# Performance work log

Hardware: AMD Instinct MI355X
Metric: run time of the kernel (lower is better)

The kernel has to match this reference:

```python
import jax, jax.numpy as jnp
import numpy as np


def _three_nn_interp(xyz1, xyz2, feat2):
    # squared Euclidean distances via gram trick, avoids (B,N,S,3) tensor
    # d2: (B, N, S)
    n1 = jnp.sum(xyz1 * xyz1, axis=-1)               # (B, N)
    n2 = jnp.sum(xyz2 * xyz2, axis=-1)               # (B, S)
    d2 = n1[:, :, None] + n2[:, None, :] - 2.0 * jnp.einsum('bnc,bsc->bns', xyz1, xyz2)
    d = jnp.sqrt(jnp.maximum(d2, 0.0))
    k = min(3, xyz2.shape[1])
    neg_d, idx = jax.lax.top_k(-d, k)                # smallest k distances
    dist = jnp.maximum(-neg_d, 1e-10)               # (B, N, k)
    w = 1.0 / dist
    w = w / jnp.sum(w, axis=-1, keepdims=True)
    # gather feat2 at idx: (B, N, k, C2)
    f2 = jnp.take_along_axis(feat2[:, None, :, :], idx[..., None], axis=2)
    return jnp.sum(f2 * w[..., None], axis=2)        # (B, N, C2)


def setup_inputs() -> dict:
    key = jax.random.key(0)
    ks = jax.random.split(key, 8)
    B, N, S, C1, C2, OUT = 8, 8192, 2048, 128, 256, 256
    IN = C1 + C2
    return {
        'xyz1': jax.random.normal(ks[0], (B, N, 3), dtype=jnp.float32),
        'xyz2': jax.random.normal(ks[1], (B, S, 3), dtype=jnp.float32),
        'feat1': jax.random.normal(ks[2], (B, N, C1), dtype=jnp.float32),
        'feat2': jax.random.normal(ks[3], (B, S, C2), dtype=jnp.float32),
        'W1': jax.random.normal(ks[4], (IN, OUT), dtype=jnp.float32) * (1.0 / np.sqrt(IN)),
        'b1': jnp.zeros((OUT,), dtype=jnp.float32),
        'W2': jax.random.normal(ks[5], (OUT, OUT), dtype=jnp.float32) * (1.0 / np.sqrt(OUT)),
        'b2': jnp.zeros((OUT,), dtype=jnp.float32),
    }


def reference(xyz1, xyz2, feat1, feat2, W1, b1, W2, b2):
    if xyz2.shape[1] == 1:
        interp = jnp.broadcast_to(feat2, (feat2.shape[0], xyz1.shape[1], feat2.shape[2]))
    else:
        interp = _three_nn_interp(xyz1, xyz2, feat2)
    x = jnp.concatenate([feat1, interp], axis=-1)    # (B, N, C1+C2)
    x = jax.nn.relu(x @ W1 + b1)
    x = jax.nn.relu(x @ W2 + b2)
    return x
```

## Files before the change

### kernel.cpp

```cpp
#include <hip/hip_runtime.h>
#include <hip/hip_bf16.h>

#define BB   8
#define NN   8192
#define SS   2048
#define C1C  128
#define C2C  256
#define KIN  384
#define OUTC 256

typedef __attribute__((ext_vector_type(4))) float f32x4;
typedef __attribute__((ext_vector_type(8))) short short8;
typedef __attribute__((ext_vector_type(8))) unsigned short ushortx8;

__device__ __forceinline__ ushort f2bf(float v) {
    __hip_bfloat16 h = __float2bfloat16(v);
    return __builtin_bit_cast(ushort, h);
}

__device__ __forceinline__ float med3(float a, float b, float c) {
    return __builtin_amdgcn_fmed3f(a, b, c);
}

__global__ __launch_bounds__(1024, 8) void knn_gather_kernel(
    const float* __restrict__ xyz1, const float* __restrict__ xyz2,
    const float* __restrict__ feat2, ushort* __restrict__ interpB)
{
    __shared__ float4 sp[SS];
    __shared__ int   sIdx[128][3];
    __shared__ float sW[128][3];

    const int tid   = threadIdx.x;
    const int b     = blockIdx.x & 7;
    const int chunk = blockIdx.x >> 3;
    const int qbase = chunk << 7;

    const float* x2 = xyz2 + (size_t)b * SS * 3;
    for (int i = tid; i < SS; i += 1024) {
        float x = x2[i*3+0], y = x2[i*3+1], z = x2[i*3+2];
        sp[i] = make_float4(-2.f*x, -2.f*y, -2.f*z, x*x + y*y + z*z);
    }
    __syncthreads();

    const int g = tid >> 4;
    const int l = tid & 15;
    const int qa = qbase + g * 2;

    const float* qp = xyz1 + ((size_t)b * NN + qa) * 3;
    float px[2] = {qp[0], qp[3]};
    float py[2] = {qp[1], qp[4]};
    float pz[2] = {qp[2], qp[5]};

    float c0[2], c1[2], c2[2];
#pragma unroll
    for (int qi = 0; qi < 2; ++qi) { c0[qi] = c1[qi] = c2[qi] = 1e30f; }

    for (int jj = 0; jj < 128; jj += 4) {
        float4 P[4];
#pragma unroll
        for (int u = 0; u < 4; ++u) P[u] = sp[((jj + u) << 4) + l];
#pragma unroll
        for (int u = 0; u < 4; ++u) {
#pragma unroll
            for (int qi = 0; qi < 2; ++qi) {
                float f = fmaf(px[qi], P[u].x,
                          fmaf(py[qi], P[u].y,
                          fmaf(pz[qi], P[u].z, P[u].w)));
                c2[qi] = med3(f, c1[qi], c2[qi]);
                c1[qi] = med3(f, c0[qi], c1[qi]);
                c0[qi] = fminf(f, c0[qi]);
            }
        }
    }

#pragma unroll
    for (int m = 1; m <= 8; m <<= 1) {
#pragma unroll
        for (int qi = 0; qi < 2; ++qi) {
            float b0 = __shfl_xor(c0[qi], m);
            float b1 = __shfl_xor(c1[qi], m);
            float b2 = __shfl_xor(c2[qi], m);
            float bv[3] = {b0, b1, b2};
#pragma unroll
            for (int e = 0; e < 3; ++e) {
                float d = bv[e];
                c2[qi] = med3(d, c1[qi], c2[qi]);
                c1[qi] = med3(d, c0[qi], c1[qi]);
                c0[qi] = fminf(d, c0[qi]);
            }
        }
    }
    const float t0 = c2[0], t1 = c2[1];

    float e0[2], e1[2], e2[2];
    int   i0[2], i1[2], i2[2];
#pragma unroll
    for (int qi = 0; qi < 2; ++qi) {
        e0[qi] = e1[qi] = e2[qi] = 1e30f;
        i0[qi] = i1[qi] = i2[qi] = 0x3fffffff;
    }

    for (int jj = 0; jj < 128; jj += 4) {
        float4 P[4];
#pragma unroll
        for (int u = 0; u < 4; ++u) P[u] = sp[((jj + u) << 4) + l];
#pragma unroll
        for (int u = 0; u < 4; ++u) {
            const int s = ((jj + u) << 4) + l;
#pragma unroll
            for (int qi = 0; qi < 2; ++qi) {
                float f = fmaf(px[qi], P[u].x,
                          fmaf(py[qi], P[u].y,
                          fmaf(pz[qi], P[u].z, P[u].w)));
                float tq = qi ? t1 : t0;
                if (f <= tq) {
                    bool lt2 = (f < e2[qi]) || (f == e2[qi] && s < i2[qi]);
                    if (lt2) {
                        bool lt1 = (f < e1[qi]) || (f == e1[qi] && s < i1[qi]);
                        bool lt0 = (f < e0[qi]) || (f == e0[qi] && s < i0[qi]);
                        e2[qi] = lt1 ? e1[qi] : f;  i2[qi] = lt1 ? i1[qi] : s;
                        e1[qi] = lt0 ? e0[qi] : (lt1 ? f : e1[qi]);
                        i1[qi] = lt0 ? i0[qi] : (lt1 ? s : i1[qi]);
                        e0[qi] = lt0 ? f : e0[qi];  i0[qi] = lt0 ? s : i0[qi];
                    }
                }
            }
        }
    }

#pragma unroll
    for (int m = 1; m <= 8; m <<= 1) {
#pragma unroll
        for (int qi = 0; qi < 2; ++qi) {
            float ob0 = __shfl_xor(e0[qi], m), ob1 = __shfl_xor(e1[qi], m), ob2 = __shfl_xor(e2[qi], m);
            int   oj0 = __shfl_xor(i0[qi], m), oj1 = __shfl_xor(i1[qi], m), oj2 = __shfl_xor(i2[qi], m);
            float dv[3] = {ob0, ob1, ob2}; int iv[3] = {oj0, oj1, oj2};
#pragma unroll
            for (int e = 0; e < 3; ++e) {
                float d = dv[e]; int s = iv[e];
                bool lt2 = (d < e2[qi]) || (d == e2[qi] && s < i2[qi]);
                if (lt2) {
                    bool lt1 = (d < e1[qi]) || (d == e1[qi] && s < i1[qi]);
                    bool lt0 = (d < e0[qi]) || (d == e0[qi] && s < i0[qi]);
                    e2[qi] = lt1 ? e1[qi] : d;  i2[qi] = lt1 ? i1[qi] : s;
                    e1[qi] = lt0 ? e0[qi] : (lt1 ? d : e1[qi]);
                    i1[qi] = lt0 ? i0[qi] : (lt1 ? s : i1[qi]);
                    e0[qi] = lt0 ? d : e0[qi];  i0[qi] = lt0 ? s : i0[qi];
                }
            }
        }
    }

    if (l == 0) {
#pragma unroll
        for (int qi = 0; qi < 2; ++qi) {
            float nx = px[qi], ny = py[qi], nz = pz[qi];
            float n1 = nx*nx + ny*ny + nz*nz;
            float d0 = sqrtf(fmaxf(n1 + e0[qi], 0.f));
            float d1 = sqrtf(fmaxf(n1 + e1[qi], 0.f));
            float d2s = sqrtf(fmaxf(n1 + e2[qi], 0.f));
            float w0 = 1.f / fmaxf(d0, 1e-10f);
            float w1 = 1.f / fmaxf(d1, 1e-10f);
            float w2 = 1.f / fmaxf(d2s, 1e-10f);
            float wsum = w0 + w1 + w2;
            int qq = g * 2 + qi;
            sIdx[qq][0] = i0[qi]; sIdx[qq][1] = i1[qi]; sIdx[qq][2] = i2[qi];
            sW[qq][0] = w0 / wsum; sW[qq][1] = w1 / wsum; sW[qq][2] = w2 / wsum;
        }
    }
    __syncthreads();

    const int wid = tid >> 6, lane = tid & 63;
    for (int qq = wid; qq < 128; qq += 16) {
        int a0 = sIdx[qq][0], a1 = sIdx[qq][1], a2 = sIdx[qq][2];
        float w0 = sW[qq][0], w1 = sW[qq][1], w2 = sW[qq][2];
        const float4* r0 = (const float4*)(feat2 + ((size_t)b * SS + a0) * C2C);
        const float4* r1 = (const float4*)(feat2 + ((size_t)b * SS + a1) * C2C);
        const float4* r2 = (const float4*)(feat2 + ((size_t)b * SS + a2) * C2C);
        float4 v0 = r0[lane], v1 = r1[lane], v2 = r2[lane];
        ushort4 o;
        o.x = f2bf(w0*v0.x + w1*v1.x + w2*v2.x);
        o.y = f2bf(w0*v0.y + w1*v1.y + w2*v2.y);
        o.z = f2bf(w0*v0.z + w1*v1.z + w2*v2.z);
        o.w = f2bf(w0*v0.w + w1*v1.w + w2*v2.w);
        *(ushort4*)(interpB + ((size_t)b * NN + qbase + qq) * C2C + lane * 4) = o;
    }
}

__global__ __launch_bounds__(256) void transpose_cvt_both_kernel(
    const float* __restrict__ W1, ushort* __restrict__ W1t,
    const float* __restrict__ W2, ushort* __restrict__ W2t)
{
    int idx = blockIdx.x * 256 + threadIdx.x;
    const int n1 = KIN * OUTC;
    if (idx < n1) {
        int n = idx / KIN, k = idx - n * KIN;
        W1t[idx] = f2bf(W1[(size_t)k * OUTC + n]);
    } else {
        int j = idx - n1;
        if (j < OUTC * OUTC) {
            int n = j / OUTC, k = j - n * OUTC;
            W2t[j] = f2bf(W2[(size_t)k * OUTC + n]);
        }
    }
}

#define GBM 128
#define GBN 256
#define GBK 32

__device__ __forceinline__ void gld_lds16(const void* g, void* l) {
    __builtin_amdgcn_global_load_lds(
        (const __attribute__((address_space(1))) void*)g,
        (__attribute__((address_space(3))) void*)l, 16, 0, 0);
}

__global__ __launch_bounds__(512, 4) void gemm_fused(
    const float* __restrict__ feat1,
    const ushort* __restrict__ interpB,
    const ushort* __restrict__ W1t, const float* __restrict__ b1,
    const ushort* __restrict__ W2t, const float* __restrict__ b2,
    float* __restrict__ out)
{
    __shared__ ushort pool[GBM * 256];
    __shared__ ushort sB2[GBN * GBK];

    ushort* sA = pool;
    ushort* sB = pool + GBM * GBK;

    const int tid  = threadIdx.x;
    const int lane = tid & 63;
    const int wid  = tid >> 6;
    const int m0   = blockIdx.x * GBM;
    const int wr   = wid >> 2;
    const int wc   = wid & 3;

    const int rsub = lane >> 2;
    const int slot = lane & 3;
    const int csub = slot * 8;
    const int usw  = (slot ^ (rsub & 3)) * 8;

    const int kgrp = (lane >> 4) * 8;
    const int rl   = lane & 15;
    const int ksw  = kgrp ^ ((rl & 3) << 3);
    const int cl   = lane & 15;
    const int rgrp = (lane >> 4) * 4;

    f32x4 acc1[4][4];
#pragma unroll
    for (int i = 0; i < 4; ++i)
#pragma unroll
        for (int j = 0; j < 4; ++j) acc1[i][j] = (f32x4){0.f, 0.f, 0.f, 0.f};

    for (int k0 = 0; k0 < KIN; k0 += GBK) {
#pragma unroll
        for (int c = 0; c < 3; ++c) {
            const int cid = wid * 3 + c;
            if (cid < 8) {
                const int r = m0 + cid * 16 + rsub;
                if (k0 < C1C) {
                    const float* src = feat1 + (size_t)r * C1C + k0 + usw;
                    float4 u = ((const float4*)src)[0];
                    float4 v = ((const float4*)src)[1];
                    ushortx8 t;
                    t[0] = f2bf(u.x); t[1] = f2bf(u.y); t[2] = f2bf(u.z); t[3] = f2bf(u.w);
                    t[4] = f2bf(v.x); t[5] = f2bf(v.y); t[6] = f2bf(v.z); t[7] = f2bf(v.w);
                    *(ushortx8*)&sA[cid * 512 + rsub * 32 + csub] = t;
                } else {
                    gld_lds16(interpB + (size_t)r * C2C + (k0 - C1C) + usw, &sA[cid * 512]);
                }
            } else {
                const int bi = cid - 8;
                const int r = bi * 16 + rsub;
                gld_lds16(W1t + (size_t)r * KIN + k0 + usw, &sB[bi * 512]);
            }
        }
        __syncthreads();

        short8 af[4], bf[4];
#pragma unroll
        for (int i = 0; i < 4; ++i) {
            af[i] = *(const short8*)&sA[(wr * 64 + i * 16 + rl) * GBK + ksw];
            bf[i] = *(const short8*)&sB[(wc * 64 + i * 16 + rl) * GBK + ksw];
        }
#pragma unroll
        for (int i = 0; i < 4; ++i)
#pragma unroll
            for (int j = 0; j < 4; ++j)
                acc1[i][j] = __builtin_amdgcn_mfma_f32_16x16x32_bf16(
                    af[i], bf[j], acc1[i][j], 0, 0, 0);
        __syncthreads();
    }

#pragma unroll
    for (int c = 0; c < 2; ++c) {
        const int cid = wid * 2 + c;
        const int r = cid * 16 + rsub;
        gld_lds16(W2t + (size_t)r * OUTC + 0 + usw, &sB2[cid * 512]);
    }

#pragma unroll
    for (int j = 0; j < 4; ++j) {
        const int c = wc * 64 + j * 16 + cl;
        const float bv = b1[c];
        const int u = c >> 3, sub = c & 7;
#pragma unroll
        for (int i = 0; i < 4; ++i) {
#pragma unroll
            for (int rr = 0; rr < 4; ++rr) {
                const int r = wr * 64 + i * 16 + rgrp + rr;
                const float v = fmaxf(acc1[i][j][rr] + bv, 0.f);
                pool[r * 256 + ((u ^ (r & 31)) << 3) + sub] = f2bf(v);
            }
        }
    }
    __syncthreads();

    f32x4 acc2[4][4];
#pragma unroll
    for (int i = 0; i < 4; ++i)
#pragma unroll
        for (int j = 0; j < 4; ++j) acc2[i][j] = (f32x4){0.f, 0.f, 0.f, 0.f};

    for (int k0 = 0; k0 < OUTC; k0 += GBK) {
        short8 af[4], bf[4];
        const int ub = (k0 >> 3) + (lane >> 4);
#pragma unroll
        for (int i = 0; i < 4; ++i) {
            const int r = wr * 64 + i * 16 + rl;
            af[i] = *(const short8*)&pool[r * 256 + ((ub ^ (r & 31)) << 3)];
            bf[i] = *(const short8*)&sB2[(wc * 64 + i * 16 + rl) * GBK + ksw];
        }
#pragma unroll
        for (int i = 0; i < 4; ++i)
#pragma unroll
            for (int j = 0; j < 4; ++j)
                acc2[i][j] = __builtin_amdgcn_mfma_f32_16x16x32_bf16(
                    af[i], bf[j], acc2[i][j], 0, 0, 0);

        const int kn = k0 + GBK;
        __syncthreads();
        if (kn < OUTC) {
#pragma unroll
            for (int c = 0; c < 2; ++c) {
                const int cid = wid * 2 + c;
                const int r = cid * 16 + rsub;
                gld_lds16(W2t + (size_t)r * OUTC + kn + usw, &sB2[cid * 512]);
            }
            __syncthreads();
        }
    }

#pragma unroll
    for (int j = 0; j < 4; ++j) {
        const int col = wc * 64 + j * 16 + cl;
        const float bv = b2[col];
#pragma unroll
        for (int i = 0; i < 4; ++i) {
            const int rowb = m0 + wr * 64 + i * 16 + rgrp;
#pragma unroll
            for (int rr = 0; rr < 4; ++rr) {
                out[(size_t)(rowb + rr) * OUTC + col] =
                    fmaxf(acc2[i][j][rr] + bv, 0.f);
            }
        }
    }
}

extern "C" void kernel_launch(void* const* d_in, const int* in_sizes, int n_in,
                              void* d_out, int out_size, void* d_ws, size_t ws_size,
                              hipStream_t stream) {
    const float* xyz1  = (const float*)d_in[0];
    const float* xyz2  = (const float*)d_in[1];
    const float* feat1 = (const float*)d_in[2];
    const float* feat2 = (const float*)d_in[3];
    const float* W1    = (const float*)d_in[4];
    const float* b1    = (const float*)d_in[5];
    const float* W2    = (const float*)d_in[6];
    const float* b2    = (const float*)d_in[7];
    float* out = (float*)d_out;

    char* ws = (char*)d_ws;
    ushort* interpB = (ushort*)(ws);
    ushort* W1t     = (ushort*)(ws + 33554432);
    ushort* W2t     = (ushort*)(ws + 33751040);

    const int M = BB * NN;

    transpose_cvt_both_kernel<<<(KIN * OUTC + OUTC * OUTC + 255) / 256, 256, 0, stream>>>(
        W1, W1t, W2, W2t);

    knn_gather_kernel<<<512, 1024, 0, stream>>>(xyz1, xyz2, feat2, interpB);

    gemm_fused<<<M / GBM, 512, 0, stream>>>(feat1, interpB, W1t, b1, W2t, b2, out);
}
```

Measured before the change: 110.7 us.

## Read weight fragments directly from global memory and double-buffer the activation tile

```diff
diff --git a/kernel.cpp b/kernel.cpp
--- a/kernel.cpp
+++ b/kernel.cpp
@@ -222,11 +222,8 @@
     const ushort* __restrict__ W2t, const float* __restrict__ b2,
     float* __restrict__ out)
 {
+    __shared__ ushort sA[2 * GBM * GBK];
     __shared__ ushort pool[GBM * 256];
-    __shared__ ushort sB2[GBN * GBK];
-
-    ushort* sA = pool;
-    ushort* sB = pool + GBM * GBK;
 
     const int tid  = threadIdx.x;
     const int lane = tid & 63;
@@ -246,57 +243,51 @@
     const int cl   = lane & 15;
     const int rgrp = (lane >> 4) * 4;
 
+    auto stageA = [&](int k0, int buf) {
+        ushort* dst = sA + buf * (GBM * GBK);
+        const int r = m0 + wid * 16 + rsub;
+        if (k0 < C1C) {
+            const float* src = feat1 + (size_t)r * C1C + k0 + usw;
+            float4 u = ((const float4*)src)[0];
+            float4 v = ((const float4*)src)[1];
+            ushortx8 t;
+            t[0] = f2bf(u.x); t[1] = f2bf(u.y); t[2] = f2bf(u.z); t[3] = f2bf(u.w);
+            t[4] = f2bf(v.x); t[5] = f2bf(v.y); t[6] = f2bf(v.z); t[7] = f2bf(v.w);
+            *(ushortx8*)&dst[wid * 512 + rsub * 32 + csub] = t;
+        } else {
+            gld_lds16(interpB + (size_t)r * C2C + (k0 - C1C) + usw, &dst[wid * 512]);
+        }
+    };
+
     f32x4 acc1[4][4];
 #pragma unroll
     for (int i = 0; i < 4; ++i)
 #pragma unroll
         for (int j = 0; j < 4; ++j) acc1[i][j] = (f32x4){0.f, 0.f, 0.f, 0.f};
 
+    int cur = 0;
+    stageA(0, 0);
     for (int k0 = 0; k0 < KIN; k0 += GBK) {
-#pragma unroll
-        for (int c = 0; c < 3; ++c) {
-            const int cid = wid * 3 + c;
-            if (cid < 8) {
-                const int r = m0 + cid * 16 + rsub;
-                if (k0 < C1C) {
-                    const float* src = feat1 + (size_t)r * C1C + k0 + usw;
-                    float4 u = ((const float4*)src)[0];
-                    float4 v = ((const float4*)src)[1];
-                    ushortx8 t;
-                    t[0] = f2bf(u.x); t[1] = f2bf(u.y); t[2] = f2bf(u.z); t[3] = f2bf(u.w);
-                    t[4] = f2bf(v.x); t[5] = f2bf(v.y); t[6] = f2bf(v.z); t[7] = f2bf(v.w);
-                    *(ushortx8*)&sA[cid * 512 + rsub * 32 + csub] = t;
-                } else {
-                    gld_lds16(interpB + (size_t)r * C2C + (k0 - C1C) + usw, &sA[cid * 512]);
-                }
-            } else {
-                const int bi = cid - 8;
-                const int r = bi * 16 + rsub;
-                gld_lds16(W1t + (size_t)r * KIN + k0 + usw, &sB[bi * 512]);
-            }
-        }
         __syncthreads();
+        if (k0 + GBK < KIN) stageA(k0 + GBK, cur ^ 1);
 
         short8 af[4], bf[4];
-#pragma unroll
-        for (int i = 0; i < 4; ++i) {
-            af[i] = *(const short8*)&sA[(wr * 64 + i * 16 + rl) * GBK + ksw];
-            bf[i] = *(const short8*)&sB[(wc * 64 + i * 16 + rl) * GBK + ksw];
-        }
+        const ushort* Wp = W1t + k0 + kgrp;
+#pragma unroll
+        for (int j = 0; j < 4; ++j)
+            bf[j] = *(const short8*)&Wp[(size_t)(wc * 64 + j * 16 + rl) * KIN];
+        const ushort* Ap = sA + cur * (GBM * GBK);
+#pragma unroll
+        for (int i = 0; i < 4; ++i)
+            af[i] = *(const short8*)&Ap[(wr * 64 + i * 16 + rl) * GBK + ksw];
+
 #pragma unroll
         for (int i = 0; i < 4; ++i)
 #pragma unroll
             for (int j = 0; j < 4; ++j)
                 acc1[i][j] = __builtin_amdgcn_mfma_f32_16x16x32_bf16(
                     af[i], bf[j], acc1[i][j], 0, 0, 0);
-        __syncthreads();
-    }
-
-#pragma unroll
-    for (int c = 0; c < 2; ++c) {
-        const int cid = wid * 2 + c;
-        const int r = cid * 16 + rsub;
-        gld_lds16(W2t + (size_t)r * OUTC + 0 + usw, &sB2[cid * 512]);
+        cur ^= 1;
     }
 
 #pragma unroll
@@ -324,12 +315,15 @@
 
     for (int k0 = 0; k0 < OUTC; k0 += GBK) {
         short8 af[4], bf[4];
+        const ushort* Wp = W2t + k0 + kgrp;
+#pragma unroll
+        for (int j = 0; j < 4; ++j)
+            bf[j] = *(const short8*)&Wp[(size_t)(wc * 64 + j * 16 + rl) * OUTC];
         const int ub = (k0 >> 3) + (lane >> 4);
 #pragma unroll
         for (int i = 0; i < 4; ++i) {
             const int r = wr * 64 + i * 16 + rl;
             af[i] = *(const short8*)&pool[r * 256 + ((ub ^ (r & 31)) << 3)];
-            bf[i] = *(const short8*)&sB2[(wc * 64 + i * 16 + rl) * GBK + ksw];
         }
 #pragma unroll
         for (int i = 0; i < 4; ++i)
@@ -337,18 +331,6 @@
             for (int j = 0; j < 4; ++j)
                 acc2[i][j] = __builtin_amdgcn_mfma_f32_16x16x32_bf16(
                     af[i], bf[j], acc2[i][j], 0, 0, 0);
-
-        const int kn = k0 + GBK;
-        __syncthreads();
-        if (kn < OUTC) {
-#pragma unroll
-            for (int c = 0; c < 2; ++c) {
-                const int cid = wid * 2 + c;
-                const int r = cid * 16 + rsub;
-                gld_lds16(W2t + (size_t)r * OUTC + kn + usw, &sB2[cid * 512]);
-            }
-            __syncthreads();
-        }
     }
 
 #pragma unroll
```

After: 118.3 us. 1.07x slower.
